# Kernel optimization log

Hardware: AMD Instinct MI355X
Metric: run time of the kernel (lower is better)

The kernel has to match this reference:

```python
import jax, jax.numpy as jnp
import numpy as np

NUM_BUCKETS = 32
MAX_DISTANCE = 128
NUM_HEADS = 16
D_KV = 64


def _relative_position_bucket(relative_position):
    # bidirectional buckets, faithful to T5Attention._relative_position_bucket
    num_buckets = NUM_BUCKETS // 2
    relative_buckets = (relative_position > 0).astype(jnp.int32) * num_buckets
    relative_position = jnp.abs(relative_position)
    max_exact = num_buckets // 2
    is_small = relative_position < max_exact
    rp_f = relative_position.astype(jnp.float32)
    rel_if_large = max_exact + (
        jnp.log(rp_f / max_exact) / np.log(MAX_DISTANCE / max_exact) * (num_buckets - max_exact)
    )
    rel_if_large = jnp.minimum(rel_if_large, num_buckets - 1)
    relative_buckets = relative_buckets + jnp.where(is_small, rp_f, rel_if_large).astype(jnp.int32)
    return relative_buckets


def setup_inputs() -> dict:
    key = jax.random.key(0)
    ks = jax.random.split(key, 6)
    B, S, D = 2, 2048, 1024
    inner = NUM_HEADS * D_KV  # 1024
    q_std = (inner * D_KV) ** (-0.5)
    kv_std = inner ** (-0.5)
    return {
        "hidden_states": jax.random.normal(ks[0], (B, S, D), jnp.float32),
        "attention_mask": jnp.ones((B, S), jnp.int32),
        "Wq": jax.random.normal(ks[1], (D, inner), jnp.float32) * q_std,
        "Wk": jax.random.normal(ks[2], (D, inner), jnp.float32) * kv_std,
        "Wv": jax.random.normal(ks[3], (D, inner), jnp.float32) * kv_std,
        "Wo": jax.random.normal(ks[4], (inner, D), jnp.float32) * kv_std,
        "rel_bias": jax.random.normal(ks[5], (NUM_BUCKETS, NUM_HEADS), jnp.float32),
    }


def reference(hidden_states, attention_mask, Wq, Wk, Wv, Wo, rel_bias):
    B, S, D = hidden_states.shape
    H, Dk = NUM_HEADS, D_KV

    q = (hidden_states @ Wq).reshape(B, S, H, Dk)
    k = (hidden_states @ Wk).reshape(B, S, H, Dk)
    v = (hidden_states @ Wv).reshape(B, S, H, Dk)
    q = q / jnp.sqrt(jnp.asarray(Dk, q.dtype))

    scores = jnp.einsum('bthd,bshd->bhts', q, k)  # [B,H,S,S]

    # relative position bias
    pos = jnp.arange(S, dtype=jnp.int32)
    rel_pos = pos[None, :] - pos[:, None]          # memory - context, [S,S]
    buckets = _relative_position_bucket(rel_pos)   # [S,S]
    bias = rel_bias[buckets]                       # [S,S,H]
    scores = scores + bias.transpose(2, 0, 1)[None].astype(scores.dtype)

    mask = attention_mask[:, None, None, :].astype(scores.dtype)
    scores = scores + (1.0 - mask) * jnp.finfo(scores.dtype).min

    attn = jax.nn.softmax(scores, axis=-1)
    out = jnp.einsum('bhts,bshd->bthd', attn, v).reshape(B, S, H * Dk)
    return out @ Wo
```

## Files before the change

kernel.cpp:

```cpp
#include <hip/hip_runtime.h>
#include <hip/hip_bf16.h>
#include <math.h>

typedef __attribute__((ext_vector_type(8))) short bf16x8;
typedef __attribute__((ext_vector_type(4))) short s16x4;
typedef __attribute__((ext_vector_type(4))) float f32x4;

constexpr int cB = 2, cS = 2048, cH = 16, cD = 64, cIn = 1024, cM = 1024;
constexpr float cLog2e = 1.4426950408889634f;

union BfPack { bf16x8 v; short s[8]; };
union BfPack4 { s16x4 v; short s[4]; };

__device__ __forceinline__ short f2bf(float f) {
    union { float f; unsigned u; } v; v.f = f;
    unsigned r = v.u + 0x7fffu + ((v.u >> 16) & 1u);
    return (short)(r >> 16);
}

__device__ __forceinline__ f32x4 mfma16(bf16x8 a, bf16x8 b, f32x4 c) {
    return __builtin_amdgcn_mfma_f32_16x16x32_bf16(a, b, c, 0, 0, 0);
}

__device__ __forceinline__ void async16(const short* g, short* l) {
    __builtin_amdgcn_global_load_lds(
        (const __attribute__((address_space(1))) unsigned*)(uintptr_t)g,
        (__attribute__((address_space(3))) unsigned*)(uintptr_t)l, 16, 0, 0);
}

__global__ void bias_table_kernel(const float* __restrict__ rel_bias,
                                  const int* __restrict__ mask,
                                  float* __restrict__ bt,
                                  float* __restrict__ maskadd) {
    int idx = blockIdx.x * blockDim.x + threadIdx.x;
    if (idx < 4096) maskadd[idx] = (1.0f - (float)mask[idx]) * -3.0e38f;
    if (idx >= 4095) return;
    int delta = idx - 2047;
    int rb = (delta > 0) ? 16 : 0;
    int ar = delta < 0 ? -delta : delta;
    int bucket;
    if (ar < 8) {
        bucket = rb + ar;
    } else {
        float rl = 8.0f + logf((float)ar * 0.125f) * 2.8853900817779268f;
        rl = fminf(rl, 15.0f);
        bucket = rb + (int)rl;
    }
    #pragma unroll
    for (int h = 0; h < cH; h++)
        bt[h * 4096 + 2048 + delta] = rel_bias[bucket * cH + h] * cLog2e;
}

__global__ __launch_bounds__(256) void conv_hidden_kernel(
    const float* __restrict__ h, short* __restrict__ hbf) {
    int t = blockIdx.x * 256 + threadIdx.x;
    const float4* src = (const float4*)h;
    float4 a = src[2 * t], b = src[2 * t + 1];
    BfPack p;
    p.s[0] = f2bf(a.x); p.s[1] = f2bf(a.y); p.s[2] = f2bf(a.z); p.s[3] = f2bf(a.w);
    p.s[4] = f2bf(b.x); p.s[5] = f2bf(b.y); p.s[6] = f2bf(b.z); p.s[7] = f2bf(b.w);
    ((bf16x8*)hbf)[t] = p.v;
}

__global__ __launch_bounds__(256) void conv_wt_kernel(
    const float* __restrict__ Wq, const float* __restrict__ Wk,
    const float* __restrict__ Wv, const float* __restrict__ Wo,
    short* __restrict__ Wt) {
    const int z = blockIdx.z;
    const float* W = (z == 0) ? Wq : (z == 1) ? Wk : (z == 2) ? Wv : Wo;
    const float scale = (z == 0) ? 0.125f * cLog2e : 1.0f;
    const int n0 = blockIdx.x * 64, k0 = blockIdx.y * 64;
    __shared__ short sW[64][72];
    const int t = threadIdx.x;
    const int r = t >> 2, c4 = (t & 3) * 16;
    {
        const float* src = W + (size_t)(k0 + r) * cM + n0 + c4;
        BfPack p[2];
        #pragma unroll
        for (int q = 0; q < 2; q++) {
            float4 x = ((const float4*)src)[2 * q];
            float4 y = ((const float4*)src)[2 * q + 1];
            p[q].s[0] = f2bf(x.x * scale); p[q].s[1] = f2bf(x.y * scale);
            p[q].s[2] = f2bf(x.z * scale); p[q].s[3] = f2bf(x.w * scale);
            p[q].s[4] = f2bf(y.x * scale); p[q].s[5] = f2bf(y.y * scale);
            p[q].s[6] = f2bf(y.z * scale); p[q].s[7] = f2bf(y.w * scale);
        }
        *(bf16x8*)&sW[r][c4] = p[0].v;
        *(bf16x8*)&sW[r][c4 + 8] = p[1].v;
    }
    __syncthreads();
    const int n = t >> 2, kc = (t & 3) * 16;
    BfPack o0, o1;
    #pragma unroll
    for (int j = 0; j < 8; j++) o0.s[j] = sW[kc + j][n];
    #pragma unroll
    for (int j = 0; j < 8; j++) o1.s[j] = sW[kc + 8 + j][n];
    short* dst = Wt + (size_t)z * cM * cIn + (size_t)(n0 + n) * cIn + k0 + kc;
    *(bf16x8*)dst = o0.v;
    *(bf16x8*)(dst + 8) = o1.v;
}

template <bool SWAP>
__device__ __forceinline__ void gemm_core(
    const short* __restrict__ A, const short* __restrict__ Bt,
    short* smem, int m0, int c0, int tid, f32x4 (&acc)[4][4]) {
    short* sA = smem;
    short* sB = smem + 4096;
    const int w = tid >> 6, l = tid & 63;
    const int m16 = l & 15, g = l >> 4;
    const int srow = l >> 2, scol = (l & 3) * 8;
    const int mq = (w & 1) * 64, nq = (w >> 1) * 64;

    for (int k0 = 0; k0 < cIn; k0 += 32) {
        __syncthreads();
        async16(A + (size_t)(m0 + w * 16 + srow) * cIn + k0 + scol,
                sA + w * 512 + l * 8);
        async16(A + (size_t)(m0 + 64 + w * 16 + srow) * cIn + k0 + scol,
                sA + 2048 + w * 512 + l * 8);
        async16(Bt + (size_t)(c0 + w * 16 + srow) * cIn + k0 + scol,
                sB + w * 512 + l * 8);
        async16(Bt + (size_t)(c0 + 64 + w * 16 + srow) * cIn + k0 + scol,
                sB + 2048 + w * 512 + l * 8);
        __syncthreads();
        bf16x8 af[4], bf[4];
        #pragma unroll
        for (int i = 0; i < 4; i++)
            af[i] = *(const bf16x8*)(sA + (mq + i * 16 + m16) * 32 + g * 8);
        #pragma unroll
        for (int j = 0; j < 4; j++)
            bf[j] = *(const bf16x8*)(sB + (nq + j * 16 + m16) * 32 + g * 8);
        #pragma unroll
        for (int i = 0; i < 4; i++)
            #pragma unroll
            for (int j = 0; j < 4; j++)
                acc[i][j] = SWAP ? mfma16(bf[j], af[i], acc[i][j])
                                 : mfma16(af[i], bf[j], acc[i][j]);
    }
}

__global__ __launch_bounds__(256) void gemm_qkv_kernel(
    const short* __restrict__ hbf, const short* __restrict__ Wt,
    short* __restrict__ Qrm, short* __restrict__ Krm, short* __restrict__ VT) {
    const int z = blockIdx.z;
    const short* Bt = Wt + (size_t)z * cM * cIn;
    const int m0 = blockIdx.y * 128, c0 = blockIdx.x * 128;
    __shared__ short smem[8192];
    const int tid = threadIdx.x, w = tid >> 6, l = tid & 63;
    const int m16 = l & 15, g = l >> 4;
    const int mq = (w & 1) * 64, nq = (w >> 1) * 64;
    f32x4 acc[4][4] = {};

    if (z <= 1) {
        gemm_core<false>(hbf, Bt, smem, m0, c0, tid, acc);
        short* dst = (z == 0) ? Qrm : Krm;
        #pragma unroll
        for (int i = 0; i < 4; i++)
            #pragma unroll
            for (int j = 0; j < 4; j++)
                #pragma unroll
                for (int r = 0; r < 4; r++)
                    dst[(size_t)(m0 + mq + i * 16 + g * 4 + r) * cM +
                        c0 + nq + j * 16 + m16] = f2bf(acc[i][j][r]);
    } else {
        gemm_core<true>(hbf, Bt, smem, m0, c0, tid, acc);
        #pragma unroll
        for (int i = 0; i < 4; i++) {
            const int srow_g = m0 + mq + i * 16 + m16;
            const int bb = srow_g >> 11, ss = srow_g & 2047;
            const int s6 = ss & 63;
            const int kap = (s6 & 3) | ((s6 & 28) << 1) | ((s6 >> 3) & 4);
            const int col = (ss & ~63) + kap;
            #pragma unroll
            for (int j = 0; j < 4; j++)
                #pragma unroll
                for (int r = 0; r < 4; r++) {
                    const int wcol = c0 + nq + j * 16 + g * 4 + r;
                    VT[(((size_t)bb * cH + (wcol >> 6)) * cD + (wcol & 63)) * cS
                       + col] = f2bf(acc[i][j][r]);
                }
        }
    }
}

__global__ __launch_bounds__(256, 2) void attn_kernel(
    const short* __restrict__ Qrm, const short* __restrict__ Krm,
    const short* __restrict__ VTK, const float* __restrict__ maskadd,
    const float* __restrict__ bias_t, short* __restrict__ ctx) {
    const int b = blockIdx.z, h = blockIdx.y;
    const int q0 = blockIdx.x * 128;
    const short* VTp = VTK + ((size_t)b * cH + h) * cS * cD;
    const float* bh = bias_t + h * 4096 + 2048;
    const float* mp = maskadd + b * cS;

    const int tid = threadIdx.x;
    const int wave = tid >> 6, lane = tid & 63;
    const int m16 = lane & 15, g = lane >> 4;

    __shared__ short Kt[2][128 * 64];
    __shared__ short Vt[2][64 * 128];

    int qv[2];
    bf16x8 qf[2][2];
    #pragma unroll
    for (int qq = 0; qq < 2; qq++) {
        qv[qq] = q0 + qq * 64 + wave * 16 + m16;
        const short* qb = Qrm + (size_t)(b * cS + qv[qq]) * cM + h * cD;
        qf[qq][0] = *(const bf16x8*)(qb + g * 8);
        qf[qq][1] = *(const bf16x8*)(qb + 32 + g * 8);
    }

    f32x4 o[2][4] = {};
    f32x4 lacc[2] = {};
    BfPack ones;
    #pragma unroll
    for (int i = 0; i < 8; i++) ones.s[i] = (short)0x3F80;

    const int u8 = tid & 7, r8 = tid >> 3;
    const int u16s = tid & 15, r16 = tid >> 4;
    const short* pK = Krm + ((size_t)b * cS + r8) * cM + h * cD +
                      ((u8 ^ (r8 & 7)) << 3);
    const short* pV = VTp + (size_t)r16 * cS + ((u16s ^ (r16 & 7)) << 3);
    short* dK = (short*)Kt + tid * 8;
    short* dV = (short*)Vt + tid * 8;

    const int kx0 = ((g ^ (m16 & 7)) << 3);
    const int kx1 = (((g + 4) ^ (m16 & 7)) << 3);

    #pragma unroll
    for (int c = 0; c < 4; c++) {
        async16(pK + (size_t)(c * 32) * cM, dK + c * 2048);
        async16(pV + (size_t)(c * 16) * cS, dV + c * 2048);
    }
    __syncthreads();

    for (int kt = 0; kt < cS; kt += 128) {
        const int buf = (kt >> 7) & 1, nxt = buf ^ 1;
        if (kt + 128 < cS) {
            #pragma unroll
            for (int c = 0; c < 4; c++) {
                async16(pK + (size_t)(kt + 128 + c * 32) * cM,
                        dK + nxt * 8192 + c * 2048);
                async16(pV + (size_t)(c * 16) * cS + kt + 128,
                        dV + nxt * 8192 + c * 2048);
            }
        }
        const short* K_ = (const short*)Kt + buf * 8192;
        const short* V_ = (const short*)Vt + buf * 8192;

        #pragma unroll
        for (int h2 = 0; h2 < 2; h2++) {
            f32x4 s[2][4];
            __builtin_amdgcn_s_setprio(1);
            #pragma unroll
            for (int t4 = 0; t4 < 4; t4++) {
                const int st = h2 * 4 + t4;
                const int keyb = kt + st * 16 + g * 4;
                bf16x8 klo = *(const bf16x8*)(K_ + (st * 16 + m16) * 64 + kx0);
                bf16x8 khi = *(const bf16x8*)(K_ + (st * 16 + m16) * 64 + kx1);
                #pragma unroll
                for (int qq = 0; qq < 2; qq++) {
                    f32x4 init;
                    #pragma unroll
                    for (int c = 0; c < 4; c++)
                        init[c] = bh[keyb + c - qv[qq]] + mp[keyb + c];
                    s[qq][t4] = mfma16(khi, qf[qq][1],
                                       mfma16(klo, qf[qq][0], init));
                }
            }
            __builtin_amdgcn_s_setprio(0);

            BfPack pp[2][2];
            #pragma unroll
            for (int qq = 0; qq < 2; qq++)
                #pragma unroll
                for (int t4 = 0; t4 < 4; t4++)
                    #pragma unroll
                    for (int r = 0; r < 2; r++) {
                        float p0 = __builtin_amdgcn_exp2f(s[qq][t4][2 * r]);
                        float p1 = __builtin_amdgcn_exp2f(s[qq][t4][2 * r + 1]);
                        __hip_bfloat162 h2v = __float22bfloat162_rn(float2{p0, p1});
                        short2 sp = *(short2*)&h2v;
                        pp[qq][t4 & 1].s[(t4 >> 1) * 4 + 2 * r]     = sp.x;
                        pp[qq][t4 & 1].s[(t4 >> 1) * 4 + 2 * r + 1] = sp.y;
                    }

            __builtin_amdgcn_s_setprio(1);
            #pragma unroll
            for (int qq = 0; qq < 2; qq++) {
                lacc[qq] = mfma16(ones.v, pp[qq][0].v, lacc[qq]);
                lacc[qq] = mfma16(ones.v, pp[qq][1].v, lacc[qq]);
            }
            #pragma unroll
            for (int nt = 0; nt < 4; nt++) {
                bf16x8 vlo = *(const bf16x8*)(V_ + (nt * 16 + m16) * 128 +
                                              h2 * 64 + kx0);
                bf16x8 vhi = *(const bf16x8*)(V_ + (nt * 16 + m16) * 128 +
                                              h2 * 64 + kx1);
                #pragma unroll
                for (int qq = 0; qq < 2; qq++) {
                    o[qq][nt] = mfma16(vlo, pp[qq][0].v, o[qq][nt]);
                    o[qq][nt] = mfma16(vhi, pp[qq][1].v, o[qq][nt]);
                }
            }
            __builtin_amdgcn_s_setprio(0);
        }

        __syncthreads();
    }

    #pragma unroll
    for (int qq = 0; qq < 2; qq++) {
        const float inv = 1.0f / lacc[qq][0];
        short* cb = ctx + (size_t)(b * cS + qv[qq]) * cM + h * cD;
        #pragma unroll
        for (int nt = 0; nt < 4; nt++) {
            BfPack4 pk;
            #pragma unroll
            for (int r = 0; r < 4; r++) pk.s[r] = f2bf(o[qq][nt][r] * inv);
            *(s16x4*)(cb + nt * 16 + g * 4) = pk.v;
        }
    }
}

__global__ __launch_bounds__(256) void gemm_o_kernel(
    const short* __restrict__ ctx, const short* __restrict__ WoT,
    float* __restrict__ out) {
    const int m0 = blockIdx.y * 128, c0 = blockIdx.x * 128;
    __shared__ short smem[8192];
    const int tid = threadIdx.x, w = tid >> 6, l = tid & 63;
    const int m16 = l & 15, g = l >> 4;
    const int mq = (w & 1) * 64, nq = (w >> 1) * 64;
    f32x4 acc[4][4] = {};
    gemm_core<false>(ctx, WoT, smem, m0, c0, tid, acc);
    #pragma unroll
    for (int i = 0; i < 4; i++)
        #pragma unroll
        for (int j = 0; j < 4; j++)
            #pragma unroll
            for (int r = 0; r < 4; r++)
                out[(size_t)(m0 + mq + i * 16 + g * 4 + r) * cM +
                    c0 + nq + j * 16 + m16] = acc[i][j][r];
}

extern "C" void kernel_launch(void* const* d_in, const int* in_sizes, int n_in,
                              void* d_out, int out_size, void* d_ws, size_t ws_size,
                              hipStream_t stream) {
    const float* hidden   = (const float*)d_in[0];
    const int*   mask     = (const int*)d_in[1];
    const float* Wq       = (const float*)d_in[2];
    const float* Wk       = (const float*)d_in[3];
    const float* Wv       = (const float*)d_in[4];
    const float* Wo       = (const float*)d_in[5];
    const float* rel_bias = (const float*)d_in[6];
    float* out = (float*)d_out;

    short* hbf_ctx = (short*)d_ws;
    short* Wt  = hbf_ctx + (size_t)4 * 1024 * 1024;
    short* Qrm = Wt  + (size_t)4 * 1024 * 1024;
    short* Krm = Qrm + (size_t)4 * 1024 * 1024;
    short* VT  = Krm + (size_t)4 * 1024 * 1024;
    float* bias_t  = (float*)(VT + (size_t)4 * 1024 * 1024);
    float* maskf   = bias_t + 16 * 4096;

    bias_table_kernel<<<16, 256, 0, stream>>>(rel_bias, mask, bias_t, maskf);
    conv_hidden_kernel<<<2048, 256, 0, stream>>>(hidden, hbf_ctx);
    conv_wt_kernel<<<dim3(16, 16, 4), 256, 0, stream>>>(Wq, Wk, Wv, Wo, Wt);
    gemm_qkv_kernel<<<dim3(8, 32, 3), 256, 0, stream>>>(hbf_ctx, Wt, Qrm, Krm, VT);
    attn_kernel<<<dim3(16, cH, cB), 256, 0, stream>>>(Qrm, Krm, VT, maskf, bias_t,
                                                      hbf_ctx);
    gemm_o_kernel<<<dim3(8, 32), 256, 0, stream>>>(hbf_ctx, Wt + (size_t)3 * 1024 * 1024,
                                                   out);
}
```

Before: 222.6 us.

## Fuse prep kernels, stage QKV epilogue via LDS, remap attention blocks, retile output GEMM

The three preprocessing kernels (bias table, hidden conversion, weight transpose) are merged into one launch to cut launch overhead. The QKV GEMM epilogue now stages results through padded shared memory so global stores are coalesced 16-byte writes, including the transposed V layout. Attention blocks are remapped so batch-heads group by XCD, and the bias/mask loads are hoisted out of the MFMA chain and added before exp2. The output GEMM uses 64-row tiles to double the block count. These changes raise LDS use and register pressure somewhat in exchange.

```diff
diff --git a/kernel.cpp b/kernel.cpp
--- a/kernel.cpp
+++ b/kernel.cpp
@@ -28,76 +28,75 @@
         (__attribute__((address_space(3))) unsigned*)(uintptr_t)l, 16, 0, 0);
 }
 
-__global__ void bias_table_kernel(const float* __restrict__ rel_bias,
-                                  const int* __restrict__ mask,
-                                  float* __restrict__ bt,
-                                  float* __restrict__ maskadd) {
-    int idx = blockIdx.x * blockDim.x + threadIdx.x;
-    if (idx < 4096) maskadd[idx] = (1.0f - (float)mask[idx]) * -3.0e38f;
-    if (idx >= 4095) return;
-    int delta = idx - 2047;
-    int rb = (delta > 0) ? 16 : 0;
-    int ar = delta < 0 ? -delta : delta;
-    int bucket;
-    if (ar < 8) {
-        bucket = rb + ar;
-    } else {
-        float rl = 8.0f + logf((float)ar * 0.125f) * 2.8853900817779268f;
-        rl = fminf(rl, 15.0f);
-        bucket = rb + (int)rl;
-    }
-    #pragma unroll
-    for (int h = 0; h < cH; h++)
-        bt[h * 4096 + 2048 + delta] = rel_bias[bucket * cH + h] * cLog2e;
-}
-
-__global__ __launch_bounds__(256) void conv_hidden_kernel(
-    const float* __restrict__ h, short* __restrict__ hbf) {
-    int t = blockIdx.x * 256 + threadIdx.x;
-    const float4* src = (const float4*)h;
-    float4 a = src[2 * t], b = src[2 * t + 1];
-    BfPack p;
-    p.s[0] = f2bf(a.x); p.s[1] = f2bf(a.y); p.s[2] = f2bf(a.z); p.s[3] = f2bf(a.w);
-    p.s[4] = f2bf(b.x); p.s[5] = f2bf(b.y); p.s[6] = f2bf(b.z); p.s[7] = f2bf(b.w);
-    ((bf16x8*)hbf)[t] = p.v;
-}
-
-__global__ __launch_bounds__(256) void conv_wt_kernel(
+__global__ __launch_bounds__(256) void prep_kernel(
+    const float* __restrict__ hidden, short* __restrict__ hbf,
     const float* __restrict__ Wq, const float* __restrict__ Wk,
     const float* __restrict__ Wv, const float* __restrict__ Wo,
-    short* __restrict__ Wt) {
-    const int z = blockIdx.z;
-    const float* W = (z == 0) ? Wq : (z == 1) ? Wk : (z == 2) ? Wv : Wo;
-    const float scale = (z == 0) ? 0.125f * cLog2e : 1.0f;
-    const int n0 = blockIdx.x * 64, k0 = blockIdx.y * 64;
-    __shared__ short sW[64][72];
-    const int t = threadIdx.x;
-    const int r = t >> 2, c4 = (t & 3) * 16;
-    {
-        const float* src = W + (size_t)(k0 + r) * cM + n0 + c4;
-        BfPack p[2];
-        #pragma unroll
-        for (int q = 0; q < 2; q++) {
-            float4 x = ((const float4*)src)[2 * q];
-            float4 y = ((const float4*)src)[2 * q + 1];
-            p[q].s[0] = f2bf(x.x * scale); p[q].s[1] = f2bf(x.y * scale);
-            p[q].s[2] = f2bf(x.z * scale); p[q].s[3] = f2bf(x.w * scale);
-            p[q].s[4] = f2bf(y.x * scale); p[q].s[5] = f2bf(y.y * scale);
-            p[q].s[6] = f2bf(y.z * scale); p[q].s[7] = f2bf(y.w * scale);
-        }
-        *(bf16x8*)&sW[r][c4] = p[0].v;
-        *(bf16x8*)&sW[r][c4 + 8] = p[1].v;
-    }
-    __syncthreads();
-    const int n = t >> 2, kc = (t & 3) * 16;
-    BfPack o0, o1;
-    #pragma unroll
-    for (int j = 0; j < 8; j++) o0.s[j] = sW[kc + j][n];
-    #pragma unroll
-    for (int j = 0; j < 8; j++) o1.s[j] = sW[kc + 8 + j][n];
-    short* dst = Wt + (size_t)z * cM * cIn + (size_t)(n0 + n) * cIn + k0 + kc;
-    *(bf16x8*)dst = o0.v;
-    *(bf16x8*)(dst + 8) = o1.v;
+    short* __restrict__ Wt,
+    const float* __restrict__ rel_bias, const int* __restrict__ mask,
+    float* __restrict__ bt, float* __restrict__ maskadd) {
+    const int bid = blockIdx.x;
+    const int tid = threadIdx.x;
+    if (bid < 2048) {
+        int t = bid * 256 + tid;
+        const float4* src = (const float4*)hidden;
+        float4 a = src[2 * t], b = src[2 * t + 1];
+        BfPack p;
+        p.s[0] = f2bf(a.x); p.s[1] = f2bf(a.y); p.s[2] = f2bf(a.z); p.s[3] = f2bf(a.w);
+        p.s[4] = f2bf(b.x); p.s[5] = f2bf(b.y); p.s[6] = f2bf(b.z); p.s[7] = f2bf(b.w);
+        ((bf16x8*)hbf)[t] = p.v;
+    } else if (bid < 3072) {
+        const int b2 = bid - 2048;
+        const int z = b2 >> 8, rem = b2 & 255;
+        const float* W = (z == 0) ? Wq : (z == 1) ? Wk : (z == 2) ? Wv : Wo;
+        const float scale = (z == 0) ? 0.125f * cLog2e : 1.0f;
+        const int n0 = (rem & 15) * 64, k0 = (rem >> 4) * 64;
+        __shared__ short sW[64][72];
+        const int r = tid >> 2, c4 = (tid & 3) * 16;
+        {
+            const float* src = W + (size_t)(k0 + r) * cM + n0 + c4;
+            BfPack p[2];
+            #pragma unroll
+            for (int q = 0; q < 2; q++) {
+                float4 x = ((const float4*)src)[2 * q];
+                float4 y = ((const float4*)src)[2 * q + 1];
+                p[q].s[0] = f2bf(x.x * scale); p[q].s[1] = f2bf(x.y * scale);
+                p[q].s[2] = f2bf(x.z * scale); p[q].s[3] = f2bf(x.w * scale);
+                p[q].s[4] = f2bf(y.x * scale); p[q].s[5] = f2bf(y.y * scale);
+                p[q].s[6] = f2bf(y.z * scale); p[q].s[7] = f2bf(y.w * scale);
+            }
+            *(bf16x8*)&sW[r][c4] = p[0].v;
+            *(bf16x8*)&sW[r][c4 + 8] = p[1].v;
+        }
+        __syncthreads();
+        const int n = tid >> 2, kc = (tid & 3) * 16;
+        BfPack o0, o1;
+        #pragma unroll
+        for (int j = 0; j < 8; j++) o0.s[j] = sW[kc + j][n];
+        #pragma unroll
+        for (int j = 0; j < 8; j++) o1.s[j] = sW[kc + 8 + j][n];
+        short* dst = Wt + (size_t)z * cM * cIn + (size_t)(n0 + n) * cIn + k0 + kc;
+        *(bf16x8*)dst = o0.v;
+        *(bf16x8*)(dst + 8) = o1.v;
+    } else {
+        int idx = (bid - 3072) * 256 + tid;
+        if (idx < 4096) maskadd[idx] = (1.0f - (float)mask[idx]) * -3.0e38f;
+        if (idx >= 4095) return;
+        int delta = idx - 2047;
+        int rb = (delta > 0) ? 16 : 0;
+        int ar = delta < 0 ? -delta : delta;
+        int bucket;
+        if (ar < 8) {
+            bucket = rb + ar;
+        } else {
+            float rl = 8.0f + logf((float)ar * 0.125f) * 2.8853900817779268f;
+            rl = fminf(rl, 15.0f);
+            bucket = rb + (int)rl;
+        }
+        #pragma unroll
+        for (int h = 0; h < cH; h++)
+            bt[h * 4096 + 2048 + delta] = rel_bias[bucket * cH + h] * cLog2e;
+    }
 }
 
 template <bool SWAP>
@@ -144,7 +143,7 @@
     const int z = blockIdx.z;
     const short* Bt = Wt + (size_t)z * cM * cIn;
     const int m0 = blockIdx.y * 128, c0 = blockIdx.x * 128;
-    __shared__ short smem[8192];
+    __shared__ short smem[128 * 132];
     const int tid = threadIdx.x, w = tid >> 6, l = tid & 63;
     const int m16 = l & 15, g = l >> 4;
     const int mq = (w & 1) * 64, nq = (w >> 1) * 64;
@@ -152,33 +151,45 @@
 
     if (z <= 1) {
         gemm_core<false>(hbf, Bt, smem, m0, c0, tid, acc);
-        short* dst = (z == 0) ? Qrm : Krm;
+        __syncthreads();
         #pragma unroll
         for (int i = 0; i < 4; i++)
             #pragma unroll
             for (int j = 0; j < 4; j++)
                 #pragma unroll
                 for (int r = 0; r < 4; r++)
-                    dst[(size_t)(m0 + mq + i * 16 + g * 4 + r) * cM +
-                        c0 + nq + j * 16 + m16] = f2bf(acc[i][j][r]);
+                    smem[(mq + i * 16 + g * 4 + r) * 132 + nq + j * 16 + m16] =
+                        f2bf(acc[i][j][r]);
+        __syncthreads();
+        const int tr = tid >> 1, hf = (tid & 1) * 64;
+        short* dst = ((z == 0) ? Qrm : Krm) + (size_t)(m0 + tr) * cM + c0 + hf;
+        #pragma unroll
+        for (int c = 0; c < 8; c++)
+            *(bf16x8*)(dst + c * 8) = *(const bf16x8*)(smem + tr * 132 + hf + c * 8);
     } else {
         gemm_core<true>(hbf, Bt, smem, m0, c0, tid, acc);
+        __syncthreads();
         #pragma unroll
         for (int i = 0; i < 4; i++) {
-            const int srow_g = m0 + mq + i * 16 + m16;
-            const int bb = srow_g >> 11, ss = srow_g & 2047;
-            const int s6 = ss & 63;
-            const int kap = (s6 & 3) | ((s6 & 28) << 1) | ((s6 >> 3) & 4);
-            const int col = (ss & ~63) + kap;
+            const int sl = mq + i * 16 + m16;
+            const int s6 = sl & 63;
+            const int pcol = (sl & 64) +
+                             ((s6 & 3) | ((s6 & 28) << 1) | ((s6 >> 3) & 4));
             #pragma unroll
             for (int j = 0; j < 4; j++)
                 #pragma unroll
-                for (int r = 0; r < 4; r++) {
-                    const int wcol = c0 + nq + j * 16 + g * 4 + r;
-                    VT[(((size_t)bb * cH + (wcol >> 6)) * cD + (wcol & 63)) * cS
-                       + col] = f2bf(acc[i][j][r]);
-                }
-        }
+                for (int r = 0; r < 4; r++)
+                    smem[(nq + j * 16 + g * 4 + r) * 132 + pcol] =
+                        f2bf(acc[i][j][r]);
+        }
+        __syncthreads();
+        const int tr = tid >> 1, hf = (tid & 1) * 64;
+        const int wcol = c0 + tr;
+        short* dst = VT + (((size_t)(m0 >> 11) * cH + (wcol >> 6)) * cD +
+                           (wcol & 63)) * cS + (m0 & 2047) + hf;
+        #pragma unroll
+        for (int c = 0; c < 8; c++)
+            *(bf16x8*)(dst + c * 8) = *(const bf16x8*)(smem + tr * 132 + hf + c * 8);
     }
 }
 
@@ -186,10 +197,15 @@
     const short* __restrict__ Qrm, const short* __restrict__ Krm,
     const short* __restrict__ VTK, const float* __restrict__ maskadd,
     const float* __restrict__ bias_t, short* __restrict__ ctx) {
-    const int b = blockIdx.z, h = blockIdx.y;
-    const int q0 = blockIdx.x * 128;
+    const int raw = blockIdx.x;
+    const int xcd = raw & 7, j = raw >> 3;
+    const int qi = j & 15, grp = j >> 4;
+    const int bh = grp * 8 + xcd;
+    const int b = bh >> 4, h = bh & 15;
+    const int q0 = qi * 128;
+
     const short* VTp = VTK + ((size_t)b * cH + h) * cS * cD;
-    const float* bh = bias_t + h * 4096 + 2048;
+    const float* bh_ = bias_t + h * 4096 + 2048;
     const float* mp = maskadd + b * cS;
 
     const int tid = threadIdx.x;
@@ -249,22 +265,29 @@
 
         #pragma unroll
         for (int h2 = 0; h2 < 2; h2++) {
+            f32x4 binit[2][4];
+            #pragma unroll
+            for (int t4 = 0; t4 < 4; t4++) {
+                const int keyb = kt + (h2 * 4 + t4) * 16 + g * 4;
+                #pragma unroll
+                for (int qq = 0; qq < 2; qq++)
+                    #pragma unroll
+                    for (int c = 0; c < 4; c++)
+                        binit[qq][t4][c] = bh_[keyb + c - qv[qq]] + mp[keyb + c];
+            }
+
             f32x4 s[2][4];
             __builtin_amdgcn_s_setprio(1);
             #pragma unroll
             for (int t4 = 0; t4 < 4; t4++) {
                 const int st = h2 * 4 + t4;
-                const int keyb = kt + st * 16 + g * 4;
                 bf16x8 klo = *(const bf16x8*)(K_ + (st * 16 + m16) * 64 + kx0);
                 bf16x8 khi = *(const bf16x8*)(K_ + (st * 16 + m16) * 64 + kx1);
                 #pragma unroll
                 for (int qq = 0; qq < 2; qq++) {
-                    f32x4 init;
-                    #pragma unroll
-                    for (int c = 0; c < 4; c++)
-                        init[c] = bh[keyb + c - qv[qq]] + mp[keyb + c];
+                    f32x4 z4 = {};
                     s[qq][t4] = mfma16(khi, qf[qq][1],
-                                       mfma16(klo, qf[qq][0], init));
+                                       mfma16(klo, qf[qq][0], z4));
                 }
             }
             __builtin_amdgcn_s_setprio(0);
@@ -276,8 +299,10 @@
                 for (int t4 = 0; t4 < 4; t4++)
                     #pragma unroll
                     for (int r = 0; r < 2; r++) {
-                        float p0 = __builtin_amdgcn_exp2f(s[qq][t4][2 * r]);
-                        float p1 = __builtin_amdgcn_exp2f(s[qq][t4][2 * r + 1]);
+                        float p0 = __builtin_amdgcn_exp2f(s[qq][t4][2 * r] +
+                                                          binit[qq][t4][2 * r]);
+                        float p1 = __builtin_amdgcn_exp2f(s[qq][t4][2 * r + 1] +
+                                                          binit[qq][t4][2 * r + 1]);
                         __hip_bfloat162 h2v = __float22bfloat162_rn(float2{p0, p1});
                         short2 sp = *(short2*)&h2v;
                         pp[qq][t4 & 1].s[(t4 >> 1) * 4 + 2 * r]     = sp.x;
@@ -325,21 +350,43 @@
 __global__ __launch_bounds__(256) void gemm_o_kernel(
     const short* __restrict__ ctx, const short* __restrict__ WoT,
     float* __restrict__ out) {
-    const int m0 = blockIdx.y * 128, c0 = blockIdx.x * 128;
-    __shared__ short smem[8192];
+    const int m0 = blockIdx.y * 64, c0 = blockIdx.x * 128;
+    __shared__ short smem[6144];
+    short* sA = smem;
+    short* sB = smem + 2048;
     const int tid = threadIdx.x, w = tid >> 6, l = tid & 63;
     const int m16 = l & 15, g = l >> 4;
-    const int mq = (w & 1) * 64, nq = (w >> 1) * 64;
-    f32x4 acc[4][4] = {};
-    gemm_core<false>(ctx, WoT, smem, m0, c0, tid, acc);
+    const int wm = (w & 1) * 32, wn = (w >> 1) * 64;
+    const int sr = tid >> 2, sc = (tid & 3) * 8;
+    f32x4 acc[2][4] = {};
+
+    for (int k0 = 0; k0 < cIn; k0 += 32) {
+        __syncthreads();
+        async16(ctx + (size_t)(m0 + (sr & 63)) * cIn + k0 + sc, sA + tid * 8);
+        async16(WoT + (size_t)(c0 + sr) * cIn + k0 + sc, sB + tid * 8);
+        async16(WoT + (size_t)(c0 + 64 + sr) * cIn + k0 + sc, sB + 2048 + tid * 8);
+        __syncthreads();
+        bf16x8 af[2], bf[4];
+        #pragma unroll
+        for (int i = 0; i < 2; i++)
+            af[i] = *(const bf16x8*)(sA + (wm + i * 16 + m16) * 32 + g * 8);
+        #pragma unroll
+        for (int jj = 0; jj < 4; jj++)
+            bf[jj] = *(const bf16x8*)(sB + (wn + jj * 16 + m16) * 32 + g * 8);
+        #pragma unroll
+        for (int i = 0; i < 2; i++)
+            #pragma unroll
+            for (int jj = 0; jj < 4; jj++)
+                acc[i][jj] = mfma16(af[i], bf[jj], acc[i][jj]);
+    }
     #pragma unroll
-    for (int i = 0; i < 4; i++)
-        #pragma unroll
-        for (int j = 0; j < 4; j++)
+    for (int i = 0; i < 2; i++)
+        #pragma unroll
+        for (int jj = 0; jj < 4; jj++)
             #pragma unroll
             for (int r = 0; r < 4; r++)
-                out[(size_t)(m0 + mq + i * 16 + g * 4 + r) * cM +
-                    c0 + nq + j * 16 + m16] = acc[i][j][r];
+                out[(size_t)(m0 + wm + i * 16 + g * 4 + r) * cM +
+                    c0 + wn + jj * 16 + m16] = acc[i][jj][r];
 }
 
 extern "C" void kernel_launch(void* const* d_in, const int* in_sizes, int n_in,
@@ -362,12 +409,10 @@
     float* bias_t  = (float*)(VT + (size_t)4 * 1024 * 1024);
     float* maskf   = bias_t + 16 * 4096;
 
-    bias_table_kernel<<<16, 256, 0, stream>>>(rel_bias, mask, bias_t, maskf);
-    conv_hidden_kernel<<<2048, 256, 0, stream>>>(hidden, hbf_ctx);
-    conv_wt_kernel<<<dim3(16, 16, 4), 256, 0, stream>>>(Wq, Wk, Wv, Wo, Wt);
+    prep_kernel<<<3088, 256, 0, stream>>>(hidden, hbf_ctx, Wq, Wk, Wv, Wo, Wt,
+                                          rel_bias, mask, bias_t, maskf);
     gemm_qkv_kernel<<<dim3(8, 32, 3), 256, 0, stream>>>(hbf_ctx, Wt, Qrm, Krm, VT);
-    attn_kernel<<<dim3(16, cH, cB), 256, 0, stream>>>(Qrm, Krm, VT, maskf, bias_t,
-                                                      hbf_ctx);
-    gemm_o_kernel<<<dim3(8, 32), 256, 0, stream>>>(hbf_ctx, Wt + (size_t)3 * 1024 * 1024,
+    attn_kernel<<<512, 256, 0, stream>>>(Qrm, Krm, VT, maskf, bias_t, hbf_ctx);
+    gemm_o_kernel<<<dim3(8, 64), 256, 0, stream>>>(hbf_ctx, Wt + (size_t)3 * 1024 * 1024,
                                                    out);
 }
```

Measured after the change: 197.1 us. 1.13x faster.
